# Kernel optimization log

Measured on AMD Instinct MI355X. Metric: run time of the kernel, lower is better.

## Reference

```python
import jax, jax.numpy as jnp
import numpy as np

KSIZE = 31
PAD = KSIZE // 2  # 15
SIGMA = 6.0
GAMMA_0 = 1.0
GAMMA_DELTA = 0.6
THRESH = 55.0


def _gabor_kernels(theta, freq):
    """Per-pixel spatially-varying Gabor kernels.
    theta, freq: [N] -> kernels [N, KSIZE, KSIZE].
    Frequency is chirped along the wave axis by freq_delta = freq/3 and the
    Gaussian aspect ratio varies from gamma_0 at the center by gamma_delta
    toward the kernel edge (matches generate_custom_gabor_torch semantics).
    """
    half = KSIZE // 2
    r = jnp.arange(-half, half + 1, dtype=jnp.float32)
    yy, xx = jnp.meshgrid(r, r, indexing='ij')  # [K,K]
    ct = jnp.cos(theta)[:, None, None]
    st = jnp.sin(theta)[:, None, None]
    x_t = xx * ct + yy * st       # along-wave coordinate
    y_t = -xx * st + yy * ct      # across-wave coordinate
    f0 = freq[:, None, None]
    f_local = f0 + (f0 / 3.0) * (y_t / half)          # freq_delta = freq/3
    gamma = GAMMA_0 + GAMMA_DELTA * jnp.abs(y_t) / half
    env = jnp.exp(-(x_t ** 2 + (gamma * y_t) ** 2) / (2.0 * SIGMA ** 2))
    return env * jnp.cos(2.0 * jnp.pi * f_local * x_t)


def _gabor_forward(fprint, freq_map, theta_map):
    H, W = fprint.shape
    i0, i1 = PAD, H - 16          # loop bounds: range(15, H-16)
    j0, j1 = PAD, W - 16
    Hout, Wout = i1 - i0, j1 - j0  # H-31, W-31 (patches always fully in-bounds)

    # [K*K, H-30, W-30] im2col patches; valid-output index 0 is center PAD.
    patches = jax.lax.conv_general_dilated_patches(
        fprint[None, None], (KSIZE, KSIZE), (1, 1), 'VALID')[0]
    patches = patches[:, :Hout, :Wout]  # centers i0..i1-1, j0..j1-1

    theta = theta_map[i0:i1, j0:j1].astype(jnp.float32) / 180.0 * jnp.pi
    freq = 0.025 + 0.0015 * freq_map[i0:i1, j0:j1].astype(jnp.float32)
    kernels = _gabor_kernels(theta.reshape(-1), freq.reshape(-1))
    kernels = kernels.reshape(Hout, Wout, KSIZE * KSIZE)

    vals = jnp.einsum('khw,hwk->hw', patches, kernels)
    out = fprint.at[i0:i1, j0:j1].set(vals)

    # normalize2Df_print_torch: shift min to 0, scale max to 100
    out = out - jnp.min(out)
    mx = jnp.max(out)
    out = jnp.where(mx != 0, out / mx * 100.0, out)
    # binarize2Df_print_torch
    return jnp.where(out > THRESH, 100.0, 0.0)


def setup_inputs() -> dict:
    key = jax.random.key(0)
    k1, k2, k3 = jax.random.split(key, 3)
    H = W = 320
    fprint = jax.random.uniform(k1, (H, W), dtype=jnp.float32) * 100.0
    freq_map = jax.random.randint(k2, (H, W), 0, 20, dtype=jnp.int32)
    theta_map = jax.random.randint(k3, (H, W), 0, 180, dtype=jnp.int32)
    return {"fprint": fprint, "freq_map": freq_map, "theta_map": theta_map}


def reference(fprint, freq_map, theta_map):
    return _gabor_forward(fprint, freq_map, theta_map)
```

## Files before the change

kernel.cpp:

```cpp
#include <hip/hip_runtime.h>
#include <math.h>

#define KS    31
#define KSP   32
#define PADV  15
#define IMG   320
#define NOUT  289
#define NTH   180
#define TABQ  (KSP * KSP)
#define RBLK  128

#define PBX   4
#define PBY   2
#define TROWS (PBY + KSP - 1)
#define TCOLS (PBX + KSP - 1)
#define TSTR  37

__global__ __launch_bounds__(256) void build_eftab(float2* __restrict__ tab) {
    const int t = blockIdx.x;
    const float th = ((float)t / 180.0f) * 3.14159265358979323846f;
    float st, ct;
    sincosf(th, &st, &ct);
    float2* base = tab + (size_t)t * TABQ;
    for (int e = threadIdx.x; e < TABQ; e += 256) {
        int dy = e >> 5, dx = e & 31;
        float2 v = make_float2(0.0f, 0.0f);
        if (dy < KS && dx < KS) {
            float y = (float)(dy - PADV);
            float x = (float)(dx - PADV);
            float x_t = fmaf(x,  ct, y * st);
            float y_t = fmaf(-x, st, y * ct);
            float gamma = fmaf(0.04f, fabsf(y_t), 1.0f);
            float gyt = gamma * y_t;
            float env = expf(-fmaf(x_t, x_t, gyt * gyt) * (1.0f / 72.0f));
            float phi = fmaf(x_t * y_t, (1.0f / 45.0f), x_t);
            v = make_float2(env, phi);
        }
        base[e] = v;
    }
}

__global__ __launch_bounds__(256) void gabor_conv(
    const float* __restrict__ fp, const int* __restrict__ fmap,
    const int* __restrict__ tmap, const float2* __restrict__ tab,
    float* __restrict__ out)
{
    __shared__ float tile[TROWS * TSTR];
    const int bh = blockIdx.y * PBY;
    const int bw = blockIdx.x * PBX;
    const int tid = threadIdx.x;

    for (int i = tid; i < TROWS * TSTR; i += 256) {
        int r = i / TSTR, c = i - r * TSTR;
        int gr = bh + r, gc = bw + c;
        tile[i] = (gr < IMG && gc < IMG) ? fp[gr * IMG + gc] : 0.0f;
    }
    __syncthreads();

    const int wave = tid >> 6, lane = tid & 63;
    const int half = lane >> 5, l = lane & 31;
    const int lr = l & 15, lh = l >> 4;
    const int pb  = wave * 2 + half;
    const int pxl = pb & 3, pyl = pb >> 2;
    const int oy = bh + pyl, ox = bw + pxl;
    const bool valid = (oy < NOUT) && (ox < NOUT);

    float acc0 = 0.0f, acc1 = 0.0f;
    if (valid) {
        const int iy = oy + PADV, ix = ox + PADV;
        const int theta = tmap[iy * IMG + ix];
        const float f0 = 0.025f + 0.0015f * (float)fmap[iy * IMG + ix];
        const float4* __restrict__ efb = (const float4*)(tab + (size_t)theta * TABQ);

        float4 tw[16];
        #pragma unroll
        for (int i = 0; i < 16; ++i) tw[i] = efb[i * 32 + l];
        #pragma unroll
        for (int i = 0; i < 16; ++i)
            asm volatile("" : "+v"(tw[i].x), "+v"(tw[i].y),
                              "+v"(tw[i].z), "+v"(tw[i].w));

        const float* tbase = &tile[pyl * TSTR + pxl + 2 * lr + lh * TSTR];
        #pragma unroll
        for (int i = 0; i < 16; ++i) {
            const float* tr = tbase + 2 * i * TSTR;
            float i0 = tr[0], i1 = tr[1];
            float w0 = tw[i].x * __builtin_amdgcn_cosf(f0 * tw[i].y);
            float w1 = tw[i].z * __builtin_amdgcn_cosf(f0 * tw[i].w);
            acc0 = fmaf(i0, w0, acc0);
            acc1 = fmaf(i1, w1, acc1);
        }
    }

    float v = acc0 + acc1;
    v += __shfl_xor(v, 1, 64);
    v += __shfl_xor(v, 2, 64);
    v += __shfl_xor(v, 4, 64);
    v += __shfl_xor(v, 8, 64);
    v += __shfl_xor(v, 16, 64);

    if (valid && l == 0)
        out[(oy + PADV) * IMG + (ox + PADV)] = v;
}

__global__ __launch_bounds__(256) void border_copy(
    const float* __restrict__ fp, float* __restrict__ out)
{
    int p = blockIdx.x * 256 + threadIdx.x;
    if (p >= IMG * IMG) return;
    int i = p / IMG, j = p - i * IMG;
    bool inner = (i >= PADV) && (i < PADV + NOUT) && (j >= PADV) && (j < PADV + NOUT);
    if (!inner) out[p] = fp[p];
}

__global__ __launch_bounds__(256) void reduce_partials(
    const float* __restrict__ out, float2* __restrict__ part)
{
    __shared__ float smin[4], smax[4];
    float vmin = INFINITY, vmax = -INFINITY;
    for (int p = blockIdx.x * 256 + threadIdx.x; p < IMG * IMG; p += RBLK * 256) {
        float v = out[p];
        vmin = fminf(vmin, v);
        vmax = fmaxf(vmax, v);
    }
    for (int off = 32; off; off >>= 1) {
        vmin = fminf(vmin, __shfl_down(vmin, off, 64));
        vmax = fmaxf(vmax, __shfl_down(vmax, off, 64));
    }
    const int wave = threadIdx.x >> 6;
    if ((threadIdx.x & 63) == 0) { smin[wave] = vmin; smax[wave] = vmax; }
    __syncthreads();
    if (threadIdx.x == 0) {
        vmin = fminf(fminf(smin[0], smin[1]), fminf(smin[2], smin[3]));
        vmax = fmaxf(fmaxf(smax[0], smax[1]), fmaxf(smax[2], smax[3]));
        part[blockIdx.x] = make_float2(vmin, vmax);
    }
}

__global__ __launch_bounds__(RBLK) void reduce_final(
    const float2* __restrict__ part, float* __restrict__ mm)
{
    __shared__ float smin[2], smax[2];
    float2 v = part[threadIdx.x];
    float vmin = v.x, vmax = v.y;
    for (int off = 32; off; off >>= 1) {
        vmin = fminf(vmin, __shfl_down(vmin, off, 64));
        vmax = fmaxf(vmax, __shfl_down(vmax, off, 64));
    }
    const int wave = threadIdx.x >> 6;
    if ((threadIdx.x & 63) == 0) { smin[wave] = vmin; smax[wave] = vmax; }
    __syncthreads();
    if (threadIdx.x == 0) {
        mm[0] = fminf(smin[0], smin[1]);
        mm[1] = fmaxf(smax[0], smax[1]);
    }
}

__global__ __launch_bounds__(256) void finalize(
    float* __restrict__ out, const float* __restrict__ mm)
{
    int p = blockIdx.x * 256 + threadIdx.x;
    if (p >= IMG * IMG) return;
    float mn = mm[0];
    float mx = mm[1] - mn;
    float v  = out[p] - mn;
    if (mx != 0.0f) v = v / mx * 100.0f;
    out[p] = (v > 55.0f) ? 100.0f : 0.0f;
}

extern "C" void kernel_launch(void* const* d_in, const int* in_sizes, int n_in,
                              void* d_out, int out_size, void* d_ws, size_t ws_size,
                              hipStream_t stream) {
    const float* fp   = (const float*)d_in[0];
    const int*   fmap = (const int*)d_in[1];
    const int*   tmap = (const int*)d_in[2];
    float* out = (float*)d_out;

    float*  mm   = (float*)d_ws;
    float2* part = (float2*)((char*)d_ws + 256);
    float2* tab  = (float2*)((char*)d_ws + 4096);

    hipLaunchKernelGGL(build_eftab, dim3(NTH), dim3(256), 0, stream, tab);

    dim3 g((NOUT + PBX - 1) / PBX, (NOUT + PBY - 1) / PBY);
    hipLaunchKernelGGL(gabor_conv, g, dim3(256), 0, stream, fp, fmap, tmap, tab, out);

    int nblk = (IMG * IMG + 255) / 256;
    hipLaunchKernelGGL(border_copy,     dim3(nblk), dim3(256), 0, stream, fp, out);
    hipLaunchKernelGGL(reduce_partials, dim3(RBLK), dim3(256), 0, stream, out, part);
    hipLaunchKernelGGL(reduce_final,    dim3(1),    dim3(RBLK), 0, stream, part, mm);
    hipLaunchKernelGGL(finalize,        dim3(nblk), dim3(256), 0, stream, out, mm);
}
```

Before: 50.65 us.

## Fuse border copy into reduce/finalize, split table build, stage weight loads

Drops the border_copy kernel: reduce_partials and finalize now read border pixels straight from the input instead of from a copied output. The table build uses four blocks per angle instead of one, one element per thread, for more parallelism. In the conv kernel the 16 weight float4 loads are issued in groups of four, each group fenced just before use, so loads overlap with compute and fewer registers are live. This saves one launch and one full-image pass, at the cost of index math in two kernels.

```diff
diff --git a/kernel.cpp b/kernel.cpp
--- a/kernel.cpp
+++ b/kernel.cpp
@@ -13,31 +13,34 @@
 #define PBX   4
 #define PBY   2
 #define TROWS (PBY + KSP - 1)
-#define TCOLS (PBX + KSP - 1)
 #define TSTR  37
 
+#define FENCE4(A,B,C,D) asm volatile("" : \
+    "+v"(A.x),"+v"(A.y),"+v"(A.z),"+v"(A.w), \
+    "+v"(B.x),"+v"(B.y),"+v"(B.z),"+v"(B.w), \
+    "+v"(C.x),"+v"(C.y),"+v"(C.z),"+v"(C.w), \
+    "+v"(D.x),"+v"(D.y),"+v"(D.z),"+v"(D.w))
+
 __global__ __launch_bounds__(256) void build_eftab(float2* __restrict__ tab) {
-    const int t = blockIdx.x;
+    const int t = blockIdx.x >> 2;
+    const int e = (blockIdx.x & 3) * 256 + threadIdx.x;
     const float th = ((float)t / 180.0f) * 3.14159265358979323846f;
     float st, ct;
     sincosf(th, &st, &ct);
-    float2* base = tab + (size_t)t * TABQ;
-    for (int e = threadIdx.x; e < TABQ; e += 256) {
-        int dy = e >> 5, dx = e & 31;
-        float2 v = make_float2(0.0f, 0.0f);
-        if (dy < KS && dx < KS) {
-            float y = (float)(dy - PADV);
-            float x = (float)(dx - PADV);
-            float x_t = fmaf(x,  ct, y * st);
-            float y_t = fmaf(-x, st, y * ct);
-            float gamma = fmaf(0.04f, fabsf(y_t), 1.0f);
-            float gyt = gamma * y_t;
-            float env = expf(-fmaf(x_t, x_t, gyt * gyt) * (1.0f / 72.0f));
-            float phi = fmaf(x_t * y_t, (1.0f / 45.0f), x_t);
-            v = make_float2(env, phi);
-        }
-        base[e] = v;
+    int dy = e >> 5, dx = e & 31;
+    float2 v = make_float2(0.0f, 0.0f);
+    if (dy < KS && dx < KS) {
+        float y = (float)(dy - PADV);
+        float x = (float)(dx - PADV);
+        float x_t = fmaf(x,  ct, y * st);
+        float y_t = fmaf(-x, st, y * ct);
+        float gamma = fmaf(0.04f, fabsf(y_t), 1.0f);
+        float gyt = gamma * y_t;
+        float env = expf(-fmaf(x_t, x_t, gyt * gyt) * (1.0f / 72.0f));
+        float phi = fmaf(x_t * y_t, (1.0f / 45.0f), x_t);
+        v = make_float2(env, phi);
     }
+    tab[(size_t)t * TABQ + e] = v;
 }
 
 __global__ __launch_bounds__(256) void gabor_conv(
@@ -71,25 +74,26 @@
         const int theta = tmap[iy * IMG + ix];
         const float f0 = 0.025f + 0.0015f * (float)fmap[iy * IMG + ix];
         const float4* __restrict__ efb = (const float4*)(tab + (size_t)theta * TABQ);
+        const float* tbase = &tile[pyl * TSTR + pxl + 2 * lr + lh * TSTR];
 
-        float4 tw[16];
-        #pragma unroll
-        for (int i = 0; i < 16; ++i) tw[i] = efb[i * 32 + l];
-        #pragma unroll
-        for (int i = 0; i < 16; ++i)
-            asm volatile("" : "+v"(tw[i].x), "+v"(tw[i].y),
-                              "+v"(tw[i].z), "+v"(tw[i].w));
+#define COMP(W,i) { const float* tr_ = tbase + 2 * (i) * TSTR;               \
+        float w0_ = W.x * __builtin_amdgcn_cosf(f0 * W.y);                   \
+        float w1_ = W.z * __builtin_amdgcn_cosf(f0 * W.w);                   \
+        acc0 = fmaf(tr_[0], w0_, acc0); acc1 = fmaf(tr_[1], w1_, acc1); }
 
-        const float* tbase = &tile[pyl * TSTR + pxl + 2 * lr + lh * TSTR];
-        #pragma unroll
-        for (int i = 0; i < 16; ++i) {
-            const float* tr = tbase + 2 * i * TSTR;
-            float i0 = tr[0], i1 = tr[1];
-            float w0 = tw[i].x * __builtin_amdgcn_cosf(f0 * tw[i].y);
-            float w1 = tw[i].z * __builtin_amdgcn_cosf(f0 * tw[i].w);
-            acc0 = fmaf(i0, w0, acc0);
-            acc1 = fmaf(i1, w1, acc1);
-        }
+        float4 a0 = efb[0*32+l], a1 = efb[1*32+l], a2 = efb[2*32+l], a3 = efb[3*32+l];
+        float4 b0 = efb[4*32+l], b1 = efb[5*32+l], b2 = efb[6*32+l], b3 = efb[7*32+l];
+        FENCE4(a0,a1,a2,a3);
+        COMP(a0,0) COMP(a1,1) COMP(a2,2) COMP(a3,3)
+        float4 c0 = efb[8*32+l], c1 = efb[9*32+l], c2 = efb[10*32+l], c3 = efb[11*32+l];
+        FENCE4(b0,b1,b2,b3);
+        COMP(b0,4) COMP(b1,5) COMP(b2,6) COMP(b3,7)
+        float4 d0 = efb[12*32+l], d1 = efb[13*32+l], d2 = efb[14*32+l], d3 = efb[15*32+l];
+        FENCE4(c0,c1,c2,c3);
+        COMP(c0,8) COMP(c1,9) COMP(c2,10) COMP(c3,11)
+        FENCE4(d0,d1,d2,d3);
+        COMP(d0,12) COMP(d1,13) COMP(d2,14) COMP(d3,15)
+#undef COMP
     }
 
     float v = acc0 + acc1;
@@ -103,23 +107,16 @@
         out[(oy + PADV) * IMG + (ox + PADV)] = v;
 }
 
-__global__ __launch_bounds__(256) void border_copy(
-    const float* __restrict__ fp, float* __restrict__ out)
-{
-    int p = blockIdx.x * 256 + threadIdx.x;
-    if (p >= IMG * IMG) return;
-    int i = p / IMG, j = p - i * IMG;
-    bool inner = (i >= PADV) && (i < PADV + NOUT) && (j >= PADV) && (j < PADV + NOUT);
-    if (!inner) out[p] = fp[p];
-}
-
 __global__ __launch_bounds__(256) void reduce_partials(
-    const float* __restrict__ out, float2* __restrict__ part)
+    const float* __restrict__ fp, const float* __restrict__ out,
+    float2* __restrict__ part)
 {
     __shared__ float smin[4], smax[4];
     float vmin = INFINITY, vmax = -INFINITY;
     for (int p = blockIdx.x * 256 + threadIdx.x; p < IMG * IMG; p += RBLK * 256) {
-        float v = out[p];
+        int i = p / IMG, j = p - i * IMG;
+        bool inner = (i >= PADV) && (i < PADV + NOUT) && (j >= PADV) && (j < PADV + NOUT);
+        float v = inner ? out[p] : fp[p];
         vmin = fminf(vmin, v);
         vmax = fmaxf(vmax, v);
     }
@@ -157,13 +154,17 @@
 }
 
 __global__ __launch_bounds__(256) void finalize(
-    float* __restrict__ out, const float* __restrict__ mm)
+    const float* __restrict__ fp, float* __restrict__ out,
+    const float* __restrict__ mm)
 {
     int p = blockIdx.x * 256 + threadIdx.x;
     if (p >= IMG * IMG) return;
+    int i = p / IMG, j = p - i * IMG;
+    bool inner = (i >= PADV) && (i < PADV + NOUT) && (j >= PADV) && (j < PADV + NOUT);
+    float raw = inner ? out[p] : fp[p];
     float mn = mm[0];
     float mx = mm[1] - mn;
-    float v  = out[p] - mn;
+    float v  = raw - mn;
     if (mx != 0.0f) v = v / mx * 100.0f;
     out[p] = (v > 55.0f) ? 100.0f : 0.0f;
 }
@@ -180,14 +181,13 @@
     float2* part = (float2*)((char*)d_ws + 256);
     float2* tab  = (float2*)((char*)d_ws + 4096);
 
-    hipLaunchKernelGGL(build_eftab, dim3(NTH), dim3(256), 0, stream, tab);
+    hipLaunchKernelGGL(build_eftab, dim3(NTH * 4), dim3(256), 0, stream, tab);
 
     dim3 g((NOUT + PBX - 1) / PBX, (NOUT + PBY - 1) / PBY);
     hipLaunchKernelGGL(gabor_conv, g, dim3(256), 0, stream, fp, fmap, tmap, tab, out);
 
     int nblk = (IMG * IMG + 255) / 256;
-    hipLaunchKernelGGL(border_copy,     dim3(nblk), dim3(256), 0, stream, fp, out);
-    hipLaunchKernelGGL(reduce_partials, dim3(RBLK), dim3(256), 0, stream, out, part);
+    hipLaunchKernelGGL(reduce_partials, dim3(RBLK), dim3(256), 0, stream, fp, out, part);
     hipLaunchKernelGGL(reduce_final,    dim3(1),    dim3(RBLK), 0, stream, part, mm);
-    hipLaunchKernelGGL(finalize,        dim3(nblk), dim3(256), 0, stream, out, mm);
+    hipLaunchKernelGGL(finalize,        dim3(nblk), dim3(256), 0, stream, fp, out, mm);
 }
```

New measurement: 46.51 us. 8.2% less time.
